# Performance work log

Measured on AMD Instinct MI355X. Metric: run time of the kernel, lower is better.

## Reference

```python
import jax, jax.numpy as jnp
import numpy as np

NEG_SLOPE = 0.2  # PyG GATConv LeakyReLU slope
BN_EPS = 1e-5
NUM_GRAPHS = 16


def gat_conv(x, src, dst, W, a_src, a_dst, bias, heads, out_c, concat):
    N = x.shape[0]
    h = (x @ W).reshape(N, heads, out_c)                      # [N,H,C]
    s_src = jnp.sum(h * a_src, axis=-1)                       # [N,H] per-node src score
    s_dst = jnp.sum(h * a_dst, axis=-1)                       # [N,H]
    e = jax.nn.leaky_relu(s_src[src] + s_dst[dst], NEG_SLOPE) # [E,H]
    # segment softmax over incoming edges of each dst node
    m = jax.ops.segment_max(e, dst, num_segments=N)           # [N,H]
    ex = jnp.exp(e - m[dst])
    denom = jax.ops.segment_sum(ex, dst, num_segments=N)      # [N,H]
    alpha = ex / (denom[dst] + 1e-16)                         # [E,H]
    msg = h[src] * alpha[:, :, None]                          # [E,H,C]
    out = jax.ops.segment_sum(msg, dst, num_segments=N)       # [N,H,C]
    out = out.reshape(N, heads * out_c) if concat else out.mean(axis=1)
    return out + bias


def batchnorm_eval(x, gamma, beta, rm, rv):
    return (x - rm) * jax.lax.rsqrt(rv + BN_EPS) * gamma + beta


def setup_inputs() -> dict:
    key = jax.random.key(0)
    ks = jax.random.split(key, 16)
    N, E, Fin, Hc, Hd, Emb = 20000, 640000, 128, 64, 4, 128
    x = jax.random.normal(ks[0], (N, Fin), dtype=jnp.float32)
    edge_index = jax.random.randint(ks[1], (2, E), 0, N, dtype=jnp.int64)
    batch = jnp.sort(jax.random.randint(ks[2], (N,), 0, NUM_GRAPHS, dtype=jnp.int64))
    sc1 = 1.0 / np.sqrt(Fin)
    sc2 = 1.0 / np.sqrt(Hc * Hd)
    return {
        "x": x, "edge_index": edge_index, "batch": batch,
        "W1": jax.random.normal(ks[3], (Fin, Hd * Hc), dtype=jnp.float32) * sc1,
        "a_src1": jax.random.normal(ks[4], (Hd, Hc), dtype=jnp.float32) * sc2,
        "a_dst1": jax.random.normal(ks[5], (Hd, Hc), dtype=jnp.float32) * sc2,
        "b1": jnp.zeros((Hd * Hc,), jnp.float32),
        "g1": jnp.ones((Hd * Hc,), jnp.float32),
        "be1": jnp.zeros((Hd * Hc,), jnp.float32),
        "rm1": jax.random.normal(ks[6], (Hd * Hc,), dtype=jnp.float32) * 0.1,
        "rv1": jnp.ones((Hd * Hc,), jnp.float32),
        "W2": jax.random.normal(ks[7], (Hd * Hc, Emb), dtype=jnp.float32) * sc2,
        "a_src2": jax.random.normal(ks[8], (1, Emb), dtype=jnp.float32) / np.sqrt(Emb),
        "a_dst2": jax.random.normal(ks[9], (1, Emb), dtype=jnp.float32) / np.sqrt(Emb),
        "b2": jnp.zeros((Emb,), jnp.float32),
        "g2": jnp.ones((Emb,), jnp.float32),
        "be2": jnp.zeros((Emb,), jnp.float32),
        "rm2": jax.random.normal(ks[10], (Emb,), dtype=jnp.float32) * 0.1,
        "rv2": jnp.ones((Emb,), jnp.float32),
    }


def reference(x, edge_index, batch, W1, a_src1, a_dst1, b1, g1, be1, rm1, rv1,
              W2, a_src2, a_dst2, b2, g2, be2, rm2, rv2):
    N = x.shape[0]
    loops = jnp.arange(N, dtype=edge_index.dtype)
    src = jnp.concatenate([edge_index[0], loops])  # PyG GATConv adds self-loops
    dst = jnp.concatenate([edge_index[1], loops])
    # layer 1: heads=4, concat
    h = gat_conv(x, src, dst, W1, a_src1, a_dst1, b1, heads=4, out_c=64, concat=True)
    h = batchnorm_eval(h, g1, be1, rm1, rv1)
    h = jax.nn.elu(h)  # dropout is identity in eval mode
    # layer 2: heads=1, no concat (mean over heads)
    h = gat_conv(h, src, dst, W2, a_src2, a_dst2, b2, heads=1, out_c=128, concat=False)
    h = batchnorm_eval(h, g2, be2, rm2, rv2)
    # global mean pool per graph
    sums = jax.ops.segment_sum(h, batch, num_segments=NUM_GRAPHS)
    cnts = jax.ops.segment_sum(jnp.ones((N,), h.dtype), batch, num_segments=NUM_GRAPHS)
    return sums / jnp.maximum(cnts, 1.0)[:, None]
```

## Files before the change

kernel.cpp:

```cpp
#include <hip/hip_runtime.h>
#include <hip/hip_bf16.h>
#include <math.h>

#define NEG_SLOPE 0.2f
#define BN_EPS 1e-5f
#define ELLW 128
#define SCLAMP 60.0f
#define LDP 68

typedef __attribute__((ext_vector_type(8))) short bf16x8;
typedef __attribute__((ext_vector_type(4))) float f32x4;

__device__ __forceinline__ void atomAddF(float* p, float v) { unsafeAtomicAdd(p, v); }
__device__ __forceinline__ float bf_lo(unsigned u) { return __uint_as_float(u << 16); }
__device__ __forceinline__ float bf_hi(unsigned u) { return __uint_as_float(u & 0xffff0000u); }
__device__ __forceinline__ float lk(float x) { return x > 0.f ? x : NEG_SLOPE * x; }
__device__ __forceinline__ float eexp(float x) { return __expf(fminf(x, SCLAMP)); }
__device__ __forceinline__ unsigned packbf(float lo, float hi) {
    return (unsigned)__bfloat16_as_ushort(__float2bfloat16(lo)) |
           ((unsigned)__bfloat16_as_ushort(__float2bfloat16(hi)) << 16);
}

__global__ __launch_bounds__(256) void prep_kernel(const float* __restrict__ x,
                                                   const float* __restrict__ W1,
                                                   const float* __restrict__ W2,
                                                   __hip_bfloat16* __restrict__ xbf,
                                                   __hip_bfloat16* __restrict__ WT1,
                                                   __hip_bfloat16* __restrict__ WT2,
                                                   int* __restrict__ zb, int zwords,
                                                   int n4) {
    int i = blockIdx.x * blockDim.x + threadIdx.x;
    if (i < n4) {
        float4 v = ((const float4*)x)[i];
        ushort4 st;
        st.x = __bfloat16_as_ushort(__float2bfloat16(v.x));
        st.y = __bfloat16_as_ushort(__float2bfloat16(v.y));
        st.z = __bfloat16_as_ushort(__float2bfloat16(v.z));
        st.w = __bfloat16_as_ushort(__float2bfloat16(v.w));
        *(ushort4*)(xbf + (size_t)i * 4) = st;
        return;
    }
    int j = i - n4;
    if (j < 128 * 256) {
        int k = j >> 8, n = j & 255;
        WT1[(size_t)n * 128 + k] = __float2bfloat16(W1[j]);
        return;
    }
    j -= 128 * 256;
    if (j < 256 * 128) {
        int k = j >> 7, n = j & 127;
        WT2[(size_t)n * 256 + k] = __float2bfloat16(W2[j]);
        return;
    }
    j -= 256 * 128;
    if (j < zwords) zb[j] = 0;
}

__device__ __forceinline__ void gemm_body(const __hip_bfloat16* __restrict__ A,
                                          const __hip_bfloat16* __restrict__ BT,
                                          __hip_bfloat16* __restrict__ C,
                                          const float* __restrict__ asrc,
                                          const float* __restrict__ adst,
                                          float* __restrict__ ssrc,
                                          float* __restrict__ sdst,
                                          int M, int N, int K, int heads,
                                          int bx, int by) {
    __shared__ __hip_bfloat16 As[64 * LDP];
    __shared__ __hip_bfloat16 Bs[64 * LDP];
    const int tid = threadIdx.x;
    const int w = tid >> 6;
    const int lane = tid & 63;
    const int q = lane >> 4;
    const int r16 = lane & 15;
    const int bm = by * 64;
    const int bn = bx * 64;
    const int lrow = tid >> 3;
    const int lseg = tid & 7;
    f32x4 acc[4] = {};

    for (int k0 = 0; k0 < K; k0 += 64) {
#pragma unroll
        for (int half = 0; half < 2; ++half) {
            int row = lrow + half * 32;
            int ga = min(bm + row, M - 1);
            *(bf16x8*)(&As[row * LDP + lseg * 8]) =
                *(const bf16x8*)(A + (size_t)ga * K + k0 + lseg * 8);
            *(bf16x8*)(&Bs[row * LDP + lseg * 8]) =
                *(const bf16x8*)(BT + (size_t)(bn + row) * K + k0 + lseg * 8);
        }
        __syncthreads();
#pragma unroll
        for (int kk = 0; kk < 64; kk += 32) {
            bf16x8 a = *(const bf16x8*)(&As[(w * 16 + r16) * LDP + kk + q * 8]);
#pragma unroll
            for (int t = 0; t < 4; ++t) {
                bf16x8 b = *(const bf16x8*)(&Bs[(t * 16 + r16) * LDP + kk + q * 8]);
                acc[t] = __builtin_amdgcn_mfma_f32_16x16x32_bf16(a, b, acc[t], 0, 0, 0);
            }
        }
        __syncthreads();
    }
    const size_t sbase = (size_t)(bn >> 6) * M * 64;
#pragma unroll
    for (int t = 0; t < 4; ++t)
#pragma unroll
        for (int r = 0; r < 4; ++r) {
            int row = bm + w * 16 + q * 4 + r;
            if (row < M)
                C[sbase + (size_t)row * 64 + t * 16 + r16] = __float2bfloat16(acc[t][r]);
        }
    if (heads) {
        const int h = (heads == 4) ? bx : 0;
        float asv[4], adv[4];
#pragma unroll
        for (int t = 0; t < 4; ++t) {
            int col = bn + t * 16 + r16;
            asv[t] = asrc[col]; adv[t] = adst[col];
        }
#pragma unroll
        for (int r = 0; r < 4; ++r) {
            int row = bm + w * 16 + q * 4 + r;
            float ss = 0.f, sd = 0.f;
#pragma unroll
            for (int t = 0; t < 4; ++t) { ss += acc[t][r] * asv[t]; sd += acc[t][r] * adv[t]; }
#pragma unroll
            for (int mask = 1; mask <= 8; mask <<= 1) {
                ss += __shfl_xor(ss, mask);
                sd += __shfl_xor(sd, mask);
            }
            if (r16 == 0 && row < M) {
                atomAddF(&ssrc[(size_t)row * heads + h], ss);
                atomAddF(&sdst[(size_t)row * heads + h], sd);
            }
        }
    }
}

__global__ __launch_bounds__(256) void sg1_kernel(const __hip_bfloat16* __restrict__ A,
                                                  const __hip_bfloat16* __restrict__ BT,
                                                  __hip_bfloat16* __restrict__ C,
                                                  const float* __restrict__ asrc,
                                                  const float* __restrict__ adst,
                                                  float* __restrict__ ssrc,
                                                  float* __restrict__ sdst,
                                                  int M, int nbg,
                                                  const int* __restrict__ src,
                                                  const int* __restrict__ dst,
                                                  int* __restrict__ cnt,
                                                  unsigned short* __restrict__ ell,
                                                  int N, int E, int Etot) {
    const int gb = blockIdx.x;
    if (gb < nbg) {
        gemm_body(A, BT, C, asrc, adst, ssrc, sdst, M, 256, 128, 4, gb & 3, gb >> 2);
        return;
    }
    const int xcd = gb & 7;
    const int sb = gb - nbg;
    const int slice = sb >> 3;
    const int nslices = (gridDim.x - nbg) >> 3;
    const int d0 = (int)((long)xcd * N / 8);
    const int d1 = (int)((long)(xcd + 1) * N / 8);
    for (int e = slice * 256 + threadIdx.x; e < Etot; e += nslices * 256) {
        int d = (e < E) ? dst[e] : e - E;
        if (d < d0 || d >= d1) continue;
        int s = (e < E) ? src[e] : d;
        int pos = atomicAdd(cnt + d, 1);
        if (pos < ELLW) ell[(size_t)d * ELLW + pos] = (unsigned short)s;
    }
}

__global__ __launch_bounds__(256) void gemm_score_kernel(const __hip_bfloat16* __restrict__ A,
                                                         const __hip_bfloat16* __restrict__ BT,
                                                         __hip_bfloat16* __restrict__ C,
                                                         const float* __restrict__ asrc,
                                                         const float* __restrict__ adst,
                                                         float* __restrict__ ssrc,
                                                         float* __restrict__ sdst,
                                                         int M, int N, int K, int heads) {
    gemm_body(A, BT, C, asrc, adst, ssrc, sdst, M, N, K, heads, blockIdx.x, blockIdx.y);
}

__global__ __launch_bounds__(256) void fused1_kernel(const unsigned short* __restrict__ ell,
                                                     const int* __restrict__ cnt,
                                                     const float* __restrict__ ssrc,
                                                     const float* __restrict__ sdst,
                                                     const __hip_bfloat16* __restrict__ h1,
                                                     const float* __restrict__ b,
                                                     const float* __restrict__ g,
                                                     const float* __restrict__ be,
                                                     const float* __restrict__ rm,
                                                     const float* __restrict__ rv,
                                                     __hip_bfloat16* __restrict__ out1,
                                                     int N) {
    __shared__ float sex[4][ELLW];
    __shared__ unsigned soff[4][ELLW];
    const int w = threadIdx.x >> 6;
    const int lane = threadIdx.x & 63;
    const int n = blockIdx.x * 4 + w;
    const int h = blockIdx.y;
    if (n >= N) return;
    const int degn = min(cnt[n], ELLW);
    const unsigned short* __restrict__ row = ell + (size_t)n * ELLW;
    const float sd = sdst[n * 4 + h];

    float den = 0.f;
    for (int i = lane; i < degn; i += 64) {
        int s = row[i];
        float e = eexp(lk(ssrc[s * 4 + h] + sd));
        sex[w][i] = e;
        soff[w][i] = (unsigned)s << 7;
        den += e;
    }
    const int degp = (degn + 15) & ~15;
    for (int i = degn + lane; i < degp; i += 64) { sex[w][i] = 0.f; soff[w][i] = 0; }
#pragma unroll
    for (int o = 32; o; o >>= 1) den += __shfl_xor(den, o);
    const float rden = 1.f / (den + 1e-16f);

    const int eg = lane >> 3;
    const int cc = lane & 7;
    const unsigned choff = (unsigned)cc * 16;
    const unsigned char* __restrict__ hb =
        (const unsigned char*)(h1 + (size_t)h * N * 64);

    float acc[8] = {};
    for (int i = 0; i < degp; i += 16) {
        int e0 = i + eg, e1 = i + 8 + eg;
        float av0 = sex[w][e0], av1 = sex[w][e1];
        unsigned o0 = soff[w][e0] + choff, o1 = soff[w][e1] + choff;
        uint4 u0 = *(const uint4*)(hb + o0);
        uint4 u1 = *(const uint4*)(hb + o1);
        acc[0] += av0 * bf_lo(u0.x); acc[1] += av0 * bf_hi(u0.x);
        acc[2] += av0 * bf_lo(u0.y); acc[3] += av0 * bf_hi(u0.y);
        acc[4] += av0 * bf_lo(u0.z); acc[5] += av0 * bf_hi(u0.z);
        acc[6] += av0 * bf_lo(u0.w); acc[7] += av0 * bf_hi(u0.w);
        acc[0] += av1 * bf_lo(u1.x); acc[1] += av1 * bf_hi(u1.x);
        acc[2] += av1 * bf_lo(u1.y); acc[3] += av1 * bf_hi(u1.y);
        acc[4] += av1 * bf_lo(u1.z); acc[5] += av1 * bf_hi(u1.z);
        acc[6] += av1 * bf_lo(u1.w); acc[7] += av1 * bf_hi(u1.w);
    }
#pragma unroll
    for (int m = 8; m <= 32; m <<= 1)
#pragma unroll
        for (int j = 0; j < 8; ++j) acc[j] += __shfl_xor(acc[j], m);

    if (eg == 0) {
        const int ch = h * 64 + cc * 8;
        float4 bb0 = *(const float4*)(b + ch),  bb1 = *(const float4*)(b + ch + 4);
        float4 gg0 = *(const float4*)(g + ch),  gg1 = *(const float4*)(g + ch + 4);
        float4 ee0 = *(const float4*)(be + ch), ee1 = *(const float4*)(be + ch + 4);
        float4 mm0 = *(const float4*)(rm + ch), mm1 = *(const float4*)(rm + ch + 4);
        float4 vv0 = *(const float4*)(rv + ch), vv1 = *(const float4*)(rv + ch + 4);
        float o0 = (acc[0] * rden + bb0.x - mm0.x) * rsqrtf(vv0.x + BN_EPS) * gg0.x + ee0.x;
        float o1 = (acc[1] * rden + bb0.y - mm0.y) * rsqrtf(vv0.y + BN_EPS) * gg0.y + ee0.y;
        float o2 = (acc[2] * rden + bb0.z - mm0.z) * rsqrtf(vv0.z + BN_EPS) * gg0.z + ee0.z;
        float o3 = (acc[3] * rden + bb0.w - mm0.w) * rsqrtf(vv0.w + BN_EPS) * gg0.w + ee0.w;
        float o4 = (acc[4] * rden + bb1.x - mm1.x) * rsqrtf(vv1.x + BN_EPS) * gg1.x + ee1.x;
        float o5 = (acc[5] * rden + bb1.y - mm1.y) * rsqrtf(vv1.y + BN_EPS) * gg1.y + ee1.y;
        float o6 = (acc[6] * rden + bb1.z - mm1.z) * rsqrtf(vv1.z + BN_EPS) * gg1.z + ee1.z;
        float o7 = (acc[7] * rden + bb1.w - mm1.w) * rsqrtf(vv1.w + BN_EPS) * gg1.w + ee1.w;
        o0 = o0 > 0.f ? o0 : expm1f(o0); o1 = o1 > 0.f ? o1 : expm1f(o1);
        o2 = o2 > 0.f ? o2 : expm1f(o2); o3 = o3 > 0.f ? o3 : expm1f(o3);
        o4 = o4 > 0.f ? o4 : expm1f(o4); o5 = o5 > 0.f ? o5 : expm1f(o5);
        o6 = o6 > 0.f ? o6 : expm1f(o6); o7 = o7 > 0.f ? o7 : expm1f(o7);
        uint4 st;
        st.x = packbf(o0, o1); st.y = packbf(o2, o3);
        st.z = packbf(o4, o5); st.w = packbf(o6, o7);
        *(uint4*)(out1 + (size_t)n * 256 + ch) = st;
    }
}

__global__ __launch_bounds__(256) void fused2_kernel(const unsigned short* __restrict__ ell,
                                                     const int* __restrict__ cnt,
                                                     const float* __restrict__ ssrc,
                                                     const float* __restrict__ sdst,
                                                     const __hip_bfloat16* __restrict__ h2,
                                                     const float* __restrict__ b,
                                                     const float* __restrict__ g,
                                                     const float* __restrict__ be,
                                                     const float* __restrict__ rm,
                                                     const float* __restrict__ rv,
                                                     __hip_bfloat16* __restrict__ out2,
                                                     int N) {
    __shared__ float sex[4][ELLW];
    __shared__ unsigned soff[4][ELLW];
    const int w = threadIdx.x >> 6;
    const int lane = threadIdx.x & 63;
    const int n = blockIdx.x * 4 + w;
    const int hf = blockIdx.y;
    if (n >= N) return;
    const int degn = min(cnt[n], ELLW);
    const unsigned short* __restrict__ row = ell + (size_t)n * ELLW;
    const float sd = sdst[n];

    float den = 0.f;
    for (int i = lane; i < degn; i += 64) {
        int s = row[i];
        float e = eexp(lk(ssrc[s] + sd));
        sex[w][i] = e;
        soff[w][i] = (unsigned)s << 7;
        den += e;
    }
    const int degp = (degn + 15) & ~15;
    for (int i = degn + lane; i < degp; i += 64) { sex[w][i] = 0.f; soff[w][i] = 0; }
#pragma unroll
    for (int o = 32; o; o >>= 1) den += __shfl_xor(den, o);
    const float rden = 1.f / (den + 1e-16f);

    const int eg = lane >> 3;
    const int cc = lane & 7;
    const unsigned choff = (unsigned)cc * 16;
    const unsigned char* __restrict__ hb =
        (const unsigned char*)(h2 + (size_t)hf * N * 64);

    float acc[8] = {};
    for (int i = 0; i < degp; i += 16) {
        int e0 = i + eg, e1 = i + 8 + eg;
        float av0 = sex[w][e0], av1 = sex[w][e1];
        unsigned o0 = soff[w][e0] + choff, o1 = soff[w][e1] + choff;
        uint4 u0 = *(const uint4*)(hb + o0);
        uint4 u1 = *(const uint4*)(hb + o1);
        acc[0] += av0 * bf_lo(u0.x); acc[1] += av0 * bf_hi(u0.x);
        acc[2] += av0 * bf_lo(u0.y); acc[3] += av0 * bf_hi(u0.y);
        acc[4] += av0 * bf_lo(u0.z); acc[5] += av0 * bf_hi(u0.z);
        acc[6] += av0 * bf_lo(u0.w); acc[7] += av0 * bf_hi(u0.w);
        acc[0] += av1 * bf_lo(u1.x); acc[1] += av1 * bf_hi(u1.x);
        acc[2] += av1 * bf_lo(u1.y); acc[3] += av1 * bf_hi(u1.y);
        acc[4] += av1 * bf_lo(u1.z); acc[5] += av1 * bf_hi(u1.z);
        acc[6] += av1 * bf_lo(u1.w); acc[7] += av1 * bf_hi(u1.w);
    }
#pragma unroll
    for (int m = 8; m <= 32; m <<= 1)
#pragma unroll
        for (int j = 0; j < 8; ++j) acc[j] += __shfl_xor(acc[j], m);

    if (eg == 0) {
        const int ch = hf * 64 + cc * 8;
        float4 bb0 = *(const float4*)(b + ch),  bb1 = *(const float4*)(b + ch + 4);
        float4 gg0 = *(const float4*)(g + ch),  gg1 = *(const float4*)(g + ch + 4);
        float4 ee0 = *(const float4*)(be + ch), ee1 = *(const float4*)(be + ch + 4);
        float4 mm0 = *(const float4*)(rm + ch), mm1 = *(const float4*)(rm + ch + 4);
        float4 vv0 = *(const float4*)(rv + ch), vv1 = *(const float4*)(rv + ch + 4);
        float o0 = (acc[0] * rden + bb0.x - mm0.x) * rsqrtf(vv0.x + BN_EPS) * gg0.x + ee0.x;
        float o1 = (acc[1] * rden + bb0.y - mm0.y) * rsqrtf(vv0.y + BN_EPS) * gg0.y + ee0.y;
        float o2 = (acc[2] * rden + bb0.z - mm0.z) * rsqrtf(vv0.z + BN_EPS) * gg0.z + ee0.z;
        float o3 = (acc[3] * rden + bb0.w - mm0.w) * rsqrtf(vv0.w + BN_EPS) * gg0.w + ee0.w;
        float o4 = (acc[4] * rden + bb1.x - mm1.x) * rsqrtf(vv1.x + BN_EPS) * gg1.x + ee1.x;
        float o5 = (acc[5] * rden + bb1.y - mm1.y) * rsqrtf(vv1.y + BN_EPS) * gg1.y + ee1.y;
        float o6 = (acc[6] * rden + bb1.z - mm1.z) * rsqrtf(vv1.z + BN_EPS) * gg1.z + ee1.z;
        float o7 = (acc[7] * rden + bb1.w - mm1.w) * rsqrtf(vv1.w + BN_EPS) * gg1.w + ee1.w;
        uint4 st;
        st.x = packbf(o0, o1); st.y = packbf(o2, o3);
        st.z = packbf(o4, o5); st.w = packbf(o6, o7);
        *(uint4*)(out2 + (size_t)n * 128 + ch) = st;
    }
}

__global__ __launch_bounds__(128) void pool_kernel(const __hip_bfloat16* __restrict__ out2,
                                                   const int* __restrict__ batch,
                                                   float* __restrict__ pool,
                                                   int N, int npb) {
    const int j = threadIdx.x;
    int n0 = blockIdx.x * npb;
    int n1 = min(n0 + npb, N);
    if (n0 >= n1) return;
    int curg = batch[n0];
    float acc = 0.f;
    for (int n = n0; n < n1; ++n) {
        int gr = batch[n];
        if (gr != curg) {
            atomAddF(pool + (size_t)curg * 128 + j, acc);
            acc = 0.f; curg = gr;
        }
        acc += __bfloat162float(out2[(size_t)n * 128 + j]);
    }
    atomAddF(pool + (size_t)curg * 128 + j, acc);
}

__device__ __forceinline__ int lowerBound(const int* __restrict__ a, int n, int v) {
    int lo = 0, hi = n;
    while (lo < hi) {
        int mid = (lo + hi) >> 1;
        if (a[mid] < v) lo = mid + 1; else hi = mid;
    }
    return lo;
}

__global__ __launch_bounds__(256) void final_kernel(const float* __restrict__ pool,
                                                    const int* __restrict__ batch,
                                                    float* __restrict__ out, int N) {
    int i = blockIdx.x * blockDim.x + threadIdx.x;
    int g = i >> 7;
    int c = lowerBound(batch, N, g + 1) - lowerBound(batch, N, g);
    out[i] = pool[i] / fmaxf((float)c, 1.f);
}

extern "C" void kernel_launch(void* const* d_in, const int* in_sizes, int n_in,
                              void* d_out, int out_size, void* d_ws, size_t ws_size,
                              hipStream_t stream) {
    const float* x    = (const float*)d_in[0];
    const int* ei     = (const int*)d_in[1];
    const int* batch  = (const int*)d_in[2];
    const float* W1   = (const float*)d_in[3];
    const float* as1  = (const float*)d_in[4];
    const float* ad1  = (const float*)d_in[5];
    const float* b1   = (const float*)d_in[6];
    const float* g1   = (const float*)d_in[7];
    const float* be1  = (const float*)d_in[8];
    const float* rm1  = (const float*)d_in[9];
    const float* rv1  = (const float*)d_in[10];
    const float* W2   = (const float*)d_in[11];
    const float* as2  = (const float*)d_in[12];
    const float* ad2  = (const float*)d_in[13];
    const float* b2   = (const float*)d_in[14];
    const float* g2   = (const float*)d_in[15];
    const float* be2  = (const float*)d_in[16];
    const float* rm2  = (const float*)d_in[17];
    const float* rv2  = (const float*)d_in[18];
    float* out = (float*)d_out;

    const int N = in_sizes[0] / 128;
    const int E = in_sizes[1] / 2;
    const int Etot = E + N;
    const int* src = ei;
    const int* dst = ei + E;

    char* p = (char*)d_ws;
    auto alloc = [&](size_t bytes) { char* r = p; p += (bytes + 255) & ~(size_t)255; return r; };
    __hip_bfloat16* h1   = (__hip_bfloat16*)alloc((size_t)N * 256 * 2);
    __hip_bfloat16* out1 = (__hip_bfloat16*)alloc((size_t)N * 256 * 2);
    __hip_bfloat16* out2 = (__hip_bfloat16*)alloc((size_t)N * 128 * 2);
    __hip_bfloat16* xbf  = (__hip_bfloat16*)alloc((size_t)N * 128 * 2);
    __hip_bfloat16* WT1  = (__hip_bfloat16*)alloc(256 * 128 * 2);
    __hip_bfloat16* WT2  = (__hip_bfloat16*)alloc(128 * 256 * 2);
    const int zwords     = N * 10 + 2048 + N;
    char* zbase          = alloc((size_t)zwords * 4);
    float* ssrc1         = (float*)zbase;
    float* sdst1         = ssrc1 + (size_t)N * 4;
    float* ssrc2         = sdst1 + (size_t)N * 4;
    float* sdst2         = ssrc2 + N;
    float* pool          = sdst2 + N;
    int*   cnt           = (int*)(pool + 2048);
    unsigned short* ell  = (unsigned short*)alloc((size_t)N * ELLW * 2);
    __hip_bfloat16* h2   = h1;

    const int n4 = N * 128 / 4;
    const int ptot = n4 + 2 * 128 * 256 + zwords;
    prep_kernel<<<(ptot + 255) / 256, 256, 0, stream>>>(x, W1, W2, xbf, WT1, WT2,
                                                        (int*)zbase, zwords, n4);

    const int nbg1 = 4 * ((N + 63) / 64);
    sg1_kernel<<<nbg1 + 2048, 256, 0, stream>>>(xbf, WT1, h1, as1, ad1, ssrc1, sdst1,
                                                N, nbg1, src, dst, cnt, ell, N, E, Etot);

    fused1_kernel<<<dim3((N + 3) / 4, 4), 256, 0, stream>>>(ell, cnt, ssrc1, sdst1, h1,
                                                            b1, g1, be1, rm1, rv1, out1, N);
    gemm_score_kernel<<<dim3(128 / 64, (N + 63) / 64), 256, 0, stream>>>(
        out1, WT2, h2, as2, ad2, ssrc2, sdst2, N, 128, 256, 1);
    fused2_kernel<<<dim3((N + 3) / 4, 2), 256, 0, stream>>>(ell, cnt, ssrc2, sdst2, h2,
                                                            b2, g2, be2, rm2, rv2, out2, N);

    pool_kernel<<<(N + 19) / 20, 128, 0, stream>>>(out2, batch, pool, N, 20);
    final_kernel<<<8, 256, 0, stream>>>(pool, batch, out, N);
}
```

Measured before the change: 256.5 us.

## Process all heads per wavefront in GAT aggregation kernels to reuse edge scores

Collapses the per-head grid dimension of both fused aggregation kernels so that each wavefront handles every head (4 in layer 1, 2 halves in layer 2) for its node. The ELL row, scores and softmax weights are loaded and exponentiated once and reused across heads, which removes redundant index loads and exp work. Edge padding shrinks from 16 to 8, and a tail step handles the leftover half-chunk. In exchange the grid has a quarter or half as many blocks and each wave does serial head loops, which lowers parallelism and latency hiding; LDS use grows for layer 1.

```diff
diff --git a/kernel.cpp b/kernel.cpp
--- a/kernel.cpp
+++ b/kernel.cpp
@@ -192,81 +192,106 @@
                                                      const float* __restrict__ rv,
                                                      __hip_bfloat16* __restrict__ out1,
                                                      int N) {
-    __shared__ float sex[4][ELLW];
+    __shared__ float sex[4][ELLW * 4];
     __shared__ unsigned soff[4][ELLW];
     const int w = threadIdx.x >> 6;
     const int lane = threadIdx.x & 63;
     const int n = blockIdx.x * 4 + w;
-    const int h = blockIdx.y;
     if (n >= N) return;
     const int degn = min(cnt[n], ELLW);
     const unsigned short* __restrict__ row = ell + (size_t)n * ELLW;
-    const float sd = sdst[n * 4 + h];
-
-    float den = 0.f;
+    const float4 sd4 = *(const float4*)(sdst + (size_t)n * 4);
+
+    float4 d4 = {0.f, 0.f, 0.f, 0.f};
     for (int i = lane; i < degn; i += 64) {
         int s = row[i];
-        float e = eexp(lk(ssrc[s * 4 + h] + sd));
-        sex[w][i] = e;
+        float4 sc = *(const float4*)(ssrc + (size_t)s * 4);
+        float4 e4;
+        e4.x = eexp(lk(sc.x + sd4.x)); e4.y = eexp(lk(sc.y + sd4.y));
+        e4.z = eexp(lk(sc.z + sd4.z)); e4.w = eexp(lk(sc.w + sd4.w));
+        *(float4*)(&sex[w][i * 4]) = e4;
         soff[w][i] = (unsigned)s << 7;
-        den += e;
-    }
-    const int degp = (degn + 15) & ~15;
-    for (int i = degn + lane; i < degp; i += 64) { sex[w][i] = 0.f; soff[w][i] = 0; }
-#pragma unroll
-    for (int o = 32; o; o >>= 1) den += __shfl_xor(den, o);
-    const float rden = 1.f / (den + 1e-16f);
+        d4.x += e4.x; d4.y += e4.y; d4.z += e4.z; d4.w += e4.w;
+    }
+    const int degp = (degn + 7) & ~7;
+    for (int i = degn + lane; i < degp; i += 64) {
+        float4 z = {0.f, 0.f, 0.f, 0.f};
+        *(float4*)(&sex[w][i * 4]) = z;
+        soff[w][i] = 0;
+    }
+#pragma unroll
+    for (int o = 32; o; o >>= 1) {
+        d4.x += __shfl_xor(d4.x, o); d4.y += __shfl_xor(d4.y, o);
+        d4.z += __shfl_xor(d4.z, o); d4.w += __shfl_xor(d4.w, o);
+    }
 
     const int eg = lane >> 3;
     const int cc = lane & 7;
     const unsigned choff = (unsigned)cc * 16;
-    const unsigned char* __restrict__ hb =
-        (const unsigned char*)(h1 + (size_t)h * N * 64);
-
-    float acc[8] = {};
-    for (int i = 0; i < degp; i += 16) {
-        int e0 = i + eg, e1 = i + 8 + eg;
-        float av0 = sex[w][e0], av1 = sex[w][e1];
-        unsigned o0 = soff[w][e0] + choff, o1 = soff[w][e1] + choff;
-        uint4 u0 = *(const uint4*)(hb + o0);
-        uint4 u1 = *(const uint4*)(hb + o1);
-        acc[0] += av0 * bf_lo(u0.x); acc[1] += av0 * bf_hi(u0.x);
-        acc[2] += av0 * bf_lo(u0.y); acc[3] += av0 * bf_hi(u0.y);
-        acc[4] += av0 * bf_lo(u0.z); acc[5] += av0 * bf_hi(u0.z);
-        acc[6] += av0 * bf_lo(u0.w); acc[7] += av0 * bf_hi(u0.w);
-        acc[0] += av1 * bf_lo(u1.x); acc[1] += av1 * bf_hi(u1.x);
-        acc[2] += av1 * bf_lo(u1.y); acc[3] += av1 * bf_hi(u1.y);
-        acc[4] += av1 * bf_lo(u1.z); acc[5] += av1 * bf_hi(u1.z);
-        acc[6] += av1 * bf_lo(u1.w); acc[7] += av1 * bf_hi(u1.w);
-    }
-#pragma unroll
-    for (int m = 8; m <= 32; m <<= 1)
-#pragma unroll
-        for (int j = 0; j < 8; ++j) acc[j] += __shfl_xor(acc[j], m);
-
-    if (eg == 0) {
-        const int ch = h * 64 + cc * 8;
-        float4 bb0 = *(const float4*)(b + ch),  bb1 = *(const float4*)(b + ch + 4);
-        float4 gg0 = *(const float4*)(g + ch),  gg1 = *(const float4*)(g + ch + 4);
-        float4 ee0 = *(const float4*)(be + ch), ee1 = *(const float4*)(be + ch + 4);
-        float4 mm0 = *(const float4*)(rm + ch), mm1 = *(const float4*)(rm + ch + 4);
-        float4 vv0 = *(const float4*)(rv + ch), vv1 = *(const float4*)(rv + ch + 4);
-        float o0 = (acc[0] * rden + bb0.x - mm0.x) * rsqrtf(vv0.x + BN_EPS) * gg0.x + ee0.x;
-        float o1 = (acc[1] * rden + bb0.y - mm0.y) * rsqrtf(vv0.y + BN_EPS) * gg0.y + ee0.y;
-        float o2 = (acc[2] * rden + bb0.z - mm0.z) * rsqrtf(vv0.z + BN_EPS) * gg0.z + ee0.z;
-        float o3 = (acc[3] * rden + bb0.w - mm0.w) * rsqrtf(vv0.w + BN_EPS) * gg0.w + ee0.w;
-        float o4 = (acc[4] * rden + bb1.x - mm1.x) * rsqrtf(vv1.x + BN_EPS) * gg1.x + ee1.x;
-        float o5 = (acc[5] * rden + bb1.y - mm1.y) * rsqrtf(vv1.y + BN_EPS) * gg1.y + ee1.y;
-        float o6 = (acc[6] * rden + bb1.z - mm1.z) * rsqrtf(vv1.z + BN_EPS) * gg1.z + ee1.z;
-        float o7 = (acc[7] * rden + bb1.w - mm1.w) * rsqrtf(vv1.w + BN_EPS) * gg1.w + ee1.w;
-        o0 = o0 > 0.f ? o0 : expm1f(o0); o1 = o1 > 0.f ? o1 : expm1f(o1);
-        o2 = o2 > 0.f ? o2 : expm1f(o2); o3 = o3 > 0.f ? o3 : expm1f(o3);
-        o4 = o4 > 0.f ? o4 : expm1f(o4); o5 = o5 > 0.f ? o5 : expm1f(o5);
-        o6 = o6 > 0.f ? o6 : expm1f(o6); o7 = o7 > 0.f ? o7 : expm1f(o7);
-        uint4 st;
-        st.x = packbf(o0, o1); st.y = packbf(o2, o3);
-        st.z = packbf(o4, o5); st.w = packbf(o6, o7);
-        *(uint4*)(out1 + (size_t)n * 256 + ch) = st;
+    const float* exw = (const float*)&sex[w][0];
+
+#pragma unroll
+    for (int h = 0; h < 4; ++h) {
+        const unsigned char* __restrict__ hb =
+            (const unsigned char*)(h1 + (size_t)h * N * 64);
+        float acc[8] = {};
+        int i = 0;
+        for (; i + 16 <= degp; i += 16) {
+            int e0 = i + eg, e1 = i + 8 + eg;
+            unsigned o0 = soff[w][e0] + choff, o1 = soff[w][e1] + choff;
+            float av0 = exw[e0 * 4 + h], av1 = exw[e1 * 4 + h];
+            uint4 u0 = *(const uint4*)(hb + o0);
+            uint4 u1 = *(const uint4*)(hb + o1);
+            acc[0] += av0 * bf_lo(u0.x); acc[1] += av0 * bf_hi(u0.x);
+            acc[2] += av0 * bf_lo(u0.y); acc[3] += av0 * bf_hi(u0.y);
+            acc[4] += av0 * bf_lo(u0.z); acc[5] += av0 * bf_hi(u0.z);
+            acc[6] += av0 * bf_lo(u0.w); acc[7] += av0 * bf_hi(u0.w);
+            acc[0] += av1 * bf_lo(u1.x); acc[1] += av1 * bf_hi(u1.x);
+            acc[2] += av1 * bf_lo(u1.y); acc[3] += av1 * bf_hi(u1.y);
+            acc[4] += av1 * bf_lo(u1.z); acc[5] += av1 * bf_hi(u1.z);
+            acc[6] += av1 * bf_lo(u1.w); acc[7] += av1 * bf_hi(u1.w);
+        }
+        if (i < degp) {
+            int e0 = i + eg;
+            unsigned o0 = soff[w][e0] + choff;
+            float av0 = exw[e0 * 4 + h];
+            uint4 u0 = *(const uint4*)(hb + o0);
+            acc[0] += av0 * bf_lo(u0.x); acc[1] += av0 * bf_hi(u0.x);
+            acc[2] += av0 * bf_lo(u0.y); acc[3] += av0 * bf_hi(u0.y);
+            acc[4] += av0 * bf_lo(u0.z); acc[5] += av0 * bf_hi(u0.z);
+            acc[6] += av0 * bf_lo(u0.w); acc[7] += av0 * bf_hi(u0.w);
+        }
+#pragma unroll
+        for (int m = 8; m <= 32; m <<= 1)
+#pragma unroll
+            for (int j = 0; j < 8; ++j) acc[j] += __shfl_xor(acc[j], m);
+
+        if (eg == 0) {
+            const float denh = h == 0 ? d4.x : h == 1 ? d4.y : h == 2 ? d4.z : d4.w;
+            const float rden = 1.f / (denh + 1e-16f);
+            const int ch = h * 64 + cc * 8;
+            float4 bb0 = *(const float4*)(b + ch),  bb1 = *(const float4*)(b + ch + 4);
+            float4 gg0 = *(const float4*)(g + ch),  gg1 = *(const float4*)(g + ch + 4);
+            float4 ee0 = *(const float4*)(be + ch), ee1 = *(const float4*)(be + ch + 4);
+            float4 mm0 = *(const float4*)(rm + ch), mm1 = *(const float4*)(rm + ch + 4);
+            float4 vv0 = *(const float4*)(rv + ch), vv1 = *(const float4*)(rv + ch + 4);
+            float o0 = (acc[0] * rden + bb0.x - mm0.x) * rsqrtf(vv0.x + BN_EPS) * gg0.x + ee0.x;
+            float o1 = (acc[1] * rden + bb0.y - mm0.y) * rsqrtf(vv0.y + BN_EPS) * gg0.y + ee0.y;
+            float o2 = (acc[2] * rden + bb0.z - mm0.z) * rsqrtf(vv0.z + BN_EPS) * gg0.z + ee0.z;
+            float o3 = (acc[3] * rden + bb0.w - mm0.w) * rsqrtf(vv0.w + BN_EPS) * gg0.w + ee0.w;
+            float o4 = (acc[4] * rden + bb1.x - mm1.x) * rsqrtf(vv1.x + BN_EPS) * gg1.x + ee1.x;
+            float o5 = (acc[5] * rden + bb1.y - mm1.y) * rsqrtf(vv1.y + BN_EPS) * gg1.y + ee1.y;
+            float o6 = (acc[6] * rden + bb1.z - mm1.z) * rsqrtf(vv1.z + BN_EPS) * gg1.z + ee1.z;
+            float o7 = (acc[7] * rden + bb1.w - mm1.w) * rsqrtf(vv1.w + BN_EPS) * gg1.w + ee1.w;
+            o0 = o0 > 0.f ? o0 : expm1f(o0); o1 = o1 > 0.f ? o1 : expm1f(o1);
+            o2 = o2 > 0.f ? o2 : expm1f(o2); o3 = o3 > 0.f ? o3 : expm1f(o3);
+            o4 = o4 > 0.f ? o4 : expm1f(o4); o5 = o5 > 0.f ? o5 : expm1f(o5);
+            o6 = o6 > 0.f ? o6 : expm1f(o6); o7 = o7 > 0.f ? o7 : expm1f(o7);
+            uint4 st;
+            st.x = packbf(o0, o1); st.y = packbf(o2, o3);
+            st.z = packbf(o4, o5); st.w = packbf(o6, o7);
+            *(uint4*)(out1 + (size_t)n * 256 + ch) = st;
+        }
     }
 }
 
@@ -287,7 +312,6 @@
     const int w = threadIdx.x >> 6;
     const int lane = threadIdx.x & 63;
     const int n = blockIdx.x * 4 + w;
-    const int hf = blockIdx.y;
     if (n >= N) return;
     const int degn = min(cnt[n], ELLW);
     const unsigned short* __restrict__ row = ell + (size_t)n * ELLW;
@@ -301,7 +325,7 @@
         soff[w][i] = (unsigned)s << 7;
         den += e;
     }
-    const int degp = (degn + 15) & ~15;
+    const int degp = (degn + 7) & ~7;
     for (int i = degn + lane; i < degp; i += 64) { sex[w][i] = 0.f; soff[w][i] = 0; }
 #pragma unroll
     for (int o = 32; o; o >>= 1) den += __shfl_xor(den, o);
@@ -310,49 +334,63 @@
     const int eg = lane >> 3;
     const int cc = lane & 7;
     const unsigned choff = (unsigned)cc * 16;
-    const unsigned char* __restrict__ hb =
-        (const unsigned char*)(h2 + (size_t)hf * N * 64);
-
-    float acc[8] = {};
-    for (int i = 0; i < degp; i += 16) {
-        int e0 = i + eg, e1 = i + 8 + eg;
-        float av0 = sex[w][e0], av1 = sex[w][e1];
-        unsigned o0 = soff[w][e0] + choff, o1 = soff[w][e1] + choff;
-        uint4 u0 = *(const uint4*)(hb + o0);
-        uint4 u1 = *(const uint4*)(hb + o1);
-        acc[0] += av0 * bf_lo(u0.x); acc[1] += av0 * bf_hi(u0.x);
-        acc[2] += av0 * bf_lo(u0.y); acc[3] += av0 * bf_hi(u0.y);
-        acc[4] += av0 * bf_lo(u0.z); acc[5] += av0 * bf_hi(u0.z);
-        acc[6] += av0 * bf_lo(u0.w); acc[7] += av0 * bf_hi(u0.w);
-        acc[0] += av1 * bf_lo(u1.x); acc[1] += av1 * bf_hi(u1.x);
-        acc[2] += av1 * bf_lo(u1.y); acc[3] += av1 * bf_hi(u1.y);
-        acc[4] += av1 * bf_lo(u1.z); acc[5] += av1 * bf_hi(u1.z);
-        acc[6] += av1 * bf_lo(u1.w); acc[7] += av1 * bf_hi(u1.w);
-    }
-#pragma unroll
-    for (int m = 8; m <= 32; m <<= 1)
-#pragma unroll
-        for (int j = 0; j < 8; ++j) acc[j] += __shfl_xor(acc[j], m);
-
-    if (eg == 0) {
-        const int ch = hf * 64 + cc * 8;
-        float4 bb0 = *(const float4*)(b + ch),  bb1 = *(const float4*)(b + ch + 4);
-        float4 gg0 = *(const float4*)(g + ch),  gg1 = *(const float4*)(g + ch + 4);
-        float4 ee0 = *(const float4*)(be + ch), ee1 = *(const float4*)(be + ch + 4);
-        float4 mm0 = *(const float4*)(rm + ch), mm1 = *(const float4*)(rm + ch + 4);
-        float4 vv0 = *(const float4*)(rv + ch), vv1 = *(const float4*)(rv + ch + 4);
-        float o0 = (acc[0] * rden + bb0.x - mm0.x) * rsqrtf(vv0.x + BN_EPS) * gg0.x + ee0.x;
-        float o1 = (acc[1] * rden + bb0.y - mm0.y) * rsqrtf(vv0.y + BN_EPS) * gg0.y + ee0.y;
-        float o2 = (acc[2] * rden + bb0.z - mm0.z) * rsqrtf(vv0.z + BN_EPS) * gg0.z + ee0.z;
-        float o3 = (acc[3] * rden + bb0.w - mm0.w) * rsqrtf(vv0.w + BN_EPS) * gg0.w + ee0.w;
-        float o4 = (acc[4] * rden + bb1.x - mm1.x) * rsqrtf(vv1.x + BN_EPS) * gg1.x + ee1.x;
-        float o5 = (acc[5] * rden + bb1.y - mm1.y) * rsqrtf(vv1.y + BN_EPS) * gg1.y + ee1.y;
-        float o6 = (acc[6] * rden + bb1.z - mm1.z) * rsqrtf(vv1.z + BN_EPS) * gg1.z + ee1.z;
-        float o7 = (acc[7] * rden + bb1.w - mm1.w) * rsqrtf(vv1.w + BN_EPS) * gg1.w + ee1.w;
-        uint4 st;
-        st.x = packbf(o0, o1); st.y = packbf(o2, o3);
-        st.z = packbf(o4, o5); st.w = packbf(o6, o7);
-        *(uint4*)(out2 + (size_t)n * 128 + ch) = st;
+
+#pragma unroll
+    for (int hf = 0; hf < 2; ++hf) {
+        const unsigned char* __restrict__ hb =
+            (const unsigned char*)(h2 + (size_t)hf * N * 64);
+        float acc[8] = {};
+        int i = 0;
+        for (; i + 16 <= degp; i += 16) {
+            int e0 = i + eg, e1 = i + 8 + eg;
+            unsigned o0 = soff[w][e0] + choff, o1 = soff[w][e1] + choff;
+            float av0 = sex[w][e0], av1 = sex[w][e1];
+            uint4 u0 = *(const uint4*)(hb + o0);
+            uint4 u1 = *(const uint4*)(hb + o1);
+            acc[0] += av0 * bf_lo(u0.x); acc[1] += av0 * bf_hi(u0.x);
+            acc[2] += av0 * bf_lo(u0.y); acc[3] += av0 * bf_hi(u0.y);
+            acc[4] += av0 * bf_lo(u0.z); acc[5] += av0 * bf_hi(u0.z);
+            acc[6] += av0 * bf_lo(u0.w); acc[7] += av0 * bf_hi(u0.w);
+            acc[0] += av1 * bf_lo(u1.x); acc[1] += av1 * bf_hi(u1.x);
+            acc[2] += av1 * bf_lo(u1.y); acc[3] += av1 * bf_hi(u1.y);
+            acc[4] += av1 * bf_lo(u1.z); acc[5] += av1 * bf_hi(u1.z);
+            acc[6] += av1 * bf_lo(u1.w); acc[7] += av1 * bf_hi(u1.w);
+        }
+        if (i < degp) {
+            int e0 = i + eg;
+            unsigned o0 = soff[w][e0] + choff;
+            float av0 = sex[w][e0];
+            uint4 u0 = *(const uint4*)(hb + o0);
+            acc[0] += av0 * bf_lo(u0.x); acc[1] += av0 * bf_hi(u0.x);
+            acc[2] += av0 * bf_lo(u0.y); acc[3] += av0 * bf_hi(u0.y);
+            acc[4] += av0 * bf_lo(u0.z); acc[5] += av0 * bf_hi(u0.z);
+            acc[6] += av0 * bf_lo(u0.w); acc[7] += av0 * bf_hi(u0.w);
+        }
+#pragma unroll
+        for (int m = 8; m <= 32; m <<= 1)
+#pragma unroll
+            for (int j = 0; j < 8; ++j) acc[j] += __shfl_xor(acc[j], m);
+
+        if (eg == 0) {
+            const int ch = hf * 64 + cc * 8;
+            float4 bb0 = *(const float4*)(b + ch),  bb1 = *(const float4*)(b + ch + 4);
+            float4 gg0 = *(const float4*)(g + ch),  gg1 = *(const float4*)(g + ch + 4);
+            float4 ee0 = *(const float4*)(be + ch), ee1 = *(const float4*)(be + ch + 4);
+            float4 mm0 = *(const float4*)(rm + ch), mm1 = *(const float4*)(rm + ch + 4);
+            float4 vv0 = *(const float4*)(rv + ch), vv1 = *(const float4*)(rv + ch + 4);
+            float o0 = (acc[0] * rden + bb0.x - mm0.x) * rsqrtf(vv0.x + BN_EPS) * gg0.x + ee0.x;
+            float o1 = (acc[1] * rden + bb0.y - mm0.y) * rsqrtf(vv0.y + BN_EPS) * gg0.y + ee0.y;
+            float o2 = (acc[2] * rden + bb0.z - mm0.z) * rsqrtf(vv0.z + BN_EPS) * gg0.z + ee0.z;
+            float o3 = (acc[3] * rden + bb0.w - mm0.w) * rsqrtf(vv0.w + BN_EPS) * gg0.w + ee0.w;
+            float o4 = (acc[4] * rden + bb1.x - mm1.x) * rsqrtf(vv1.x + BN_EPS) * gg1.x + ee1.x;
+            float o5 = (acc[5] * rden + bb1.y - mm1.y) * rsqrtf(vv1.y + BN_EPS) * gg1.y + ee1.y;
+            float o6 = (acc[6] * rden + bb1.z - mm1.z) * rsqrtf(vv1.z + BN_EPS) * gg1.z + ee1.z;
+            float o7 = (acc[7] * rden + bb1.w - mm1.w) * rsqrtf(vv1.w + BN_EPS) * gg1.w + ee1.w;
+            uint4 st;
+            st.x = packbf(o0, o1); st.y = packbf(o2, o3);
+            st.z = packbf(o4, o5); st.w = packbf(o6, o7);
+            *(uint4*)(out2 + (size_t)n * 128 + ch) = st;
+        }
     }
 }
 
@@ -453,12 +491,12 @@
     sg1_kernel<<<nbg1 + 2048, 256, 0, stream>>>(xbf, WT1, h1, as1, ad1, ssrc1, sdst1,
                                                 N, nbg1, src, dst, cnt, ell, N, E, Etot);
 
-    fused1_kernel<<<dim3((N + 3) / 4, 4), 256, 0, stream>>>(ell, cnt, ssrc1, sdst1, h1,
-                                                            b1, g1, be1, rm1, rv1, out1, N);
+    fused1_kernel<<<(N + 3) / 4, 256, 0, stream>>>(ell, cnt, ssrc1, sdst1, h1,
+                                                   b1, g1, be1, rm1, rv1, out1, N);
     gemm_score_kernel<<<dim3(128 / 64, (N + 63) / 64), 256, 0, stream>>>(
         out1, WT2, h2, as2, ad2, ssrc2, sdst2, N, 128, 256, 1);
-    fused2_kernel<<<dim3((N + 3) / 4, 2), 256, 0, stream>>>(ell, cnt, ssrc2, sdst2, h2,
-                                                            b2, g2, be2, rm2, rv2, out2, N);
+    fused2_kernel<<<(N + 3) / 4, 256, 0, stream>>>(ell, cnt, ssrc2, sdst2, h2,
+                                                   b2, g2, be2, rm2, rv2, out2, N);
 
     pool_kernel<<<(N + 19) / 20, 128, 0, stream>>>(out2, batch, pool, N, 20);
     final_kernel<<<8, 256, 0, stream>>>(pool, batch, out, N);
```

Result: no change. 257.6 us (+0.4%).
